# Optimization experiments

Hardware: AMD Instinct MI355X
Metric: run time of the kernel (lower is better)

The kernel has to match this reference:

```python
import jax, jax.numpy as jnp
from jax import lax
import numpy as np

L, B, D_IN, D_OUT, D_MLP = 64, 32, 512, 512, 128
WINDOWS = [1, 3]
FEATS = [256, 128]
C = sum(FEATS)  # 384
EPS = 1e-5


def _leaky(x):
    return jnp.where(x >= 0, x, 0.1 * x)


def setup_inputs() -> dict:
    key = jax.random.key(0)
    ks = jax.random.split(key, 16)
    s = lambda k, shp: (jax.random.normal(k, shp, jnp.float32) * 0.02)
    inp = {}
    inp["x"] = jax.random.normal(ks[0], (L, B, D_IN), jnp.float32)
    inp["xs_mask"] = jnp.ones((L, B), jnp.float32)
    # conv + batchnorm params per window
    inp["conv_w0"] = s(ks[1], (FEATS[0], 1, D_IN * WINDOWS[0]))
    inp["conv_b0"] = jnp.zeros((FEATS[0],), jnp.float32)
    inp["gamma0"] = jnp.ones((FEATS[0],), jnp.float32)
    inp["beta0"] = jnp.zeros((FEATS[0],), jnp.float32)
    inp["conv_w1"] = s(ks[2], (FEATS[1], 1, D_IN * WINDOWS[1]))
    inp["conv_b1"] = jnp.zeros((FEATS[1],), jnp.float32)
    inp["gamma1"] = jnp.ones((FEATS[1],), jnp.float32)
    inp["beta1"] = jnp.zeros((FEATS[1],), jnp.float32)
    inp["w0"] = s(ks[3], (2 * C, D_MLP)); inp["b0"] = jnp.zeros((D_MLP,), jnp.float32)
    inp["w1"] = s(ks[4], (D_MLP, D_MLP)); inp["b1"] = jnp.zeros((D_MLP,), jnp.float32)
    inp["w2"] = s(ks[5], (D_MLP, D_MLP)); inp["b2"] = jnp.zeros((D_MLP,), jnp.float32)
    inp["w3"] = s(ks[6], (D_MLP, D_MLP)); inp["b3"] = jnp.zeros((D_MLP,), jnp.float32)
    # output MLP: Linear(d_mlp->d_mlp), Linear(d_mlp->d_out)
    inp["w4"] = s(ks[7], (D_MLP, D_MLP)); inp["b4"] = jnp.zeros((D_MLP,), jnp.float32)
    inp["w5"] = s(ks[8], (D_MLP, D_OUT)); inp["b5"] = jnp.zeros((D_OUT,), jnp.float32)
    return inp


def reference(x, xs_mask, conv_w0, conv_b0, gamma0, beta0, conv_w1, conv_b1,
              gamma1, beta1, w0, b0, w1, b1, w2, b2, w3, b3, w4, b4, w5, b5):
    # x: (L, B, E)
    x = x * xs_mask[:, :, None]
    xf = jnp.transpose(x, (1, 0, 2)).reshape(B, 1, L * D_IN)  # (B, 1, L*E)

    # CNN front-end: Conv1d(stride=d_in) + BatchNorm1d (batch stats) + LeakyReLU
    feats = []
    for win, cw, cb, g, bt in [(WINDOWS[0], conv_w0, conv_b0, gamma0, beta0),
                               (WINDOWS[1], conv_w1, conv_b1, gamma1, beta1)]:
        pad = (win - 1) // 2 * D_IN
        y = lax.conv_general_dilated(xf, cw, window_strides=(D_IN,),
                                     padding=[(pad, pad)],
                                     dimension_numbers=("NCH", "OIH", "NCH"))
        y = y + cb[None, :, None]  # (B, C_k, L)
        m = y.mean(axis=(0, 2))
        v = y.var(axis=(0, 2))  # biased var, as torch BN training mode
        y = (y - m[None, :, None]) / jnp.sqrt(v[None, :, None] + EPS)
        y = y * g[None, :, None] + bt[None, :, None]
        feats.append(_leaky(y))
    h = jnp.concatenate(feats, axis=1)          # (B, C, L)
    h = jnp.transpose(h, (2, 0, 1))             # (L, B, C)
    h = h * xs_mask[:, :, None]

    # Graph propagation: pairwise concat + first linear, split over concat halves
    # cat([h_i, h_j]) @ w0 == h_i @ w0[:C] + h_j @ w0[C:]  (avoids (L,L,B,2C) tensor)
    a = jnp.einsum("lbc,cd->lbd", h, w0[:C])    # (L, B, d_mlp)
    bb = jnp.einsum("lbc,cd->lbd", h, w0[C:])   # (L, B, d_mlp)
    p = _leaky(a[:, None, :, :] + bb[None, :, :, :] + b0)  # (L, L, B, d_mlp)
    p = _leaky(p @ w1 + b1)
    p = _leaky(p @ w2 + b2)
    p = _leaky(p @ w3 + b3)
    p = p * xs_mask[:, None, :, None]
    p = p.mean(axis=1)                          # (L, B, d_mlp)

    out = _leaky(p @ w4 + b4)
    out = _leaky(out @ w5 + b5)                 # (L, B, d_out)
    return out * xs_mask[:, :, None]
```

## Files before the change

### kernel.cpp

```cpp
#include <hip/hip_runtime.h>


#define BB 32
#define CCH 384

__device__ __forceinline__ float leaky(float x) { return fmaxf(x, 0.1f * x); }

typedef _Float16 f16x8 __attribute__((ext_vector_type(8)));
typedef float f32x4 __attribute__((ext_vector_type(4)));

union F8 { uint4 q; f16x8 h; };
union H2 { _Float16 f[2]; uint32_t u; };

__device__ __forceinline__ void split2(float d0, float d1,
                                       uint32_t& hw, uint32_t& lw) {
  H2 h, l;
  h.f[0] = (_Float16)d0; h.f[1] = (_Float16)d1;
  l.f[0] = (_Float16)((d0 - (float)h.f[0]) * 2048.0f);
  l.f[1] = (_Float16)((d1 - (float)h.f[1]) * 2048.0f);
  hw = h.u; lw = l.u;
}

__global__ __launch_bounds__(256) void conv_kernel(
    const float* __restrict__ x, const float* __restrict__ mask,
    const float* __restrict__ cw0, const float* __restrict__ cw1,
    float* __restrict__ yG, float* __restrict__ Ssum, float* __restrict__ Ssq)
{
  __shared__ uint32_t Ah[64 * 68], Al[64 * 68];
  __shared__ uint32_t Bh[64 * 68], Bl[64 * 68];
  int bx = blockIdx.x;
  int nb = bx % 6, mb = bx / 6;
  int n0 = nb * 64;
  int row0 = mb * 64;
  bool w3 = (nb >= 4);
  int nch = w3 ? 12 : 4;
  const float* wbase = w3 ? (cw1 + (n0 - 256) * 1536) : (cw0 + n0 * 512);
  int wK = w3 ? 1536 : 512;

  int tid = threadIdx.x;
  int wid = __builtin_amdgcn_readfirstlane(tid >> 6);
  int wm = wid & 1, wn2 = wid >> 1;
  int lane = tid & 63;
  int m16 = lane & 15, q = lane >> 4;

  f32x4 hi[2][2], cr[2][2];
#pragma unroll
  for (int a = 0; a < 2; ++a)
#pragma unroll
    for (int b = 0; b < 2; ++b) {
      hi[a][b] = (f32x4){0.f, 0.f, 0.f, 0.f};
      cr[a][b] = (f32x4){0.f, 0.f, 0.f, 0.f};
    }

#pragma unroll 1
  for (int ch = 0; ch < nch; ++ch) {
    int kg0 = ch * 128;
    int tap = kg0 >> 9;
    int d0 = kg0 & 511;
    int shift = w3 ? (tap - 1) * 32 : 0;
    __syncthreads();
#pragma unroll 1
    for (int it = 0; it < 4; ++it) {
      int idx = it * 256 + tid;
      int r = idx >> 4;
      int k8 = (idx & 15) * 8;
      float d[8];
      int rowg = row0 + r + shift;
      if ((unsigned)rowg < 2048u) {
        float mv = mask[rowg];
        const float* xp = x + rowg * 512 + d0 + k8;
        float4 a0 = *(const float4*)xp;
        float4 a1 = *(const float4*)(xp + 4);
        d[0] = a0.x * mv; d[1] = a0.y * mv; d[2] = a0.z * mv; d[3] = a0.w * mv;
        d[4] = a1.x * mv; d[5] = a1.y * mv; d[6] = a1.z * mv; d[7] = a1.w * mv;
      } else {
#pragma unroll
        for (int t2 = 0; t2 < 8; ++t2) d[t2] = 0.f;
      }
      uint4 hq, lq;
      split2(d[0], d[1], hq.x, lq.x);
      split2(d[2], d[3], hq.y, lq.y);
      split2(d[4], d[5], hq.z, lq.z);
      split2(d[6], d[7], hq.w, lq.w);
      *(uint4*)&Ah[r * 68 + k8 / 2] = hq;
      *(uint4*)&Al[r * 68 + k8 / 2] = lq;
      const float* wp = wbase + r * wK + kg0 + k8;
      float4 b0v = *(const float4*)wp;
      float4 b1v = *(const float4*)(wp + 4);
      split2(b0v.x, b0v.y, hq.x, lq.x);
      split2(b0v.z, b0v.w, hq.y, lq.y);
      split2(b1v.x, b1v.y, hq.z, lq.z);
      split2(b1v.z, b1v.w, hq.w, lq.w);
      *(uint4*)&Bh[r * 68 + k8 / 2] = hq;
      *(uint4*)&Bl[r * 68 + k8 / 2] = lq;
    }
    __syncthreads();
#pragma unroll
    for (int ks = 0; ks < 4; ++ks) {
      int koff = ks * 16 + q * 4;
      F8 bh[2], bl[2];
#pragma unroll
      for (int nt = 0; nt < 2; ++nt) {
        int br = wn2 * 32 + nt * 16 + m16;
        bh[nt].q = *(const uint4*)&Bh[br * 68 + koff];
        bl[nt].q = *(const uint4*)&Bl[br * 68 + koff];
      }
#pragma unroll
      for (int mt = 0; mt < 2; ++mt) {
        int ar = wm * 32 + mt * 16 + m16;
        F8 ah, al;
        ah.q = *(const uint4*)&Ah[ar * 68 + koff];
        al.q = *(const uint4*)&Al[ar * 68 + koff];
#pragma unroll
        for (int nt = 0; nt < 2; ++nt) {
          hi[mt][nt] = __builtin_amdgcn_mfma_f32_16x16x32_f16(
              ah.h, bh[nt].h, hi[mt][nt], 0, 0, 0);
          cr[mt][nt] = __builtin_amdgcn_mfma_f32_16x16x32_f16(
              ah.h, bl[nt].h, cr[mt][nt], 0, 0, 0);
          cr[mt][nt] = __builtin_amdgcn_mfma_f32_16x16x32_f16(
              al.h, bh[nt].h, cr[mt][nt], 0, 0, 0);
        }
      }
    }
  }

  float y[2][2][4];
#pragma unroll
  for (int mt = 0; mt < 2; ++mt)
#pragma unroll
    for (int nt = 0; nt < 2; ++nt)
#pragma unroll
      for (int rg = 0; rg < 4; ++rg)
        y[mt][nt][rg] = hi[mt][nt][rg] + cr[mt][nt][rg] * (1.0f / 2048.0f);

#pragma unroll
  for (int nt = 0; nt < 2; ++nt) {
    float s = 0.f, s2 = 0.f;
#pragma unroll
    for (int mt = 0; mt < 2; ++mt)
#pragma unroll
      for (int rg = 0; rg < 4; ++rg) {
        float v = y[mt][nt][rg];
        s += v; s2 += v * v;
      }
    s  += __shfl_xor(s, 16, 64);  s  += __shfl_xor(s, 32, 64);
    s2 += __shfl_xor(s2, 16, 64); s2 += __shfl_xor(s2, 32, 64);
    if (lane < 16) {
      int c = n0 + wn2 * 32 + nt * 16 + m16;
      atomicAdd(&Ssum[c], s);
      atomicAdd(&Ssq[c], s2);
    }
  }

  __syncthreads();
  float* Yl = (float*)Ah;
#pragma unroll
  for (int mt = 0; mt < 2; ++mt)
#pragma unroll
    for (int nt = 0; nt < 2; ++nt)
#pragma unroll
      for (int rg = 0; rg < 4; ++rg)
        Yl[(wn2 * 32 + nt * 16 + m16) * 68 + wm * 32 + mt * 16 + q * 4 + rg] =
            y[mt][nt][rg];
  __syncthreads();
  {
    int c = tid >> 2, seg = (tid & 3) * 16;
#pragma unroll
    for (int j = 0; j < 16; j += 4)
      *(float4*)&yG[(n0 + c) * 2048 + row0 + seg + j] =
          *(const float4*)&Yl[c * 68 + seg + j];
  }
}

__global__ __launch_bounds__(256) void ab_kernel(
    const float* __restrict__ yG, const float* __restrict__ Ssum,
    const float* __restrict__ Ssq,
    const float* __restrict__ g0, const float* __restrict__ be0,
    const float* __restrict__ g1, const float* __restrict__ be1,
    const float* __restrict__ mask, const float* __restrict__ w0,
    const float* __restrict__ w1, const float* __restrict__ w2,
    const float* __restrict__ w3, uint32_t* __restrict__ wpk,
    float* __restrict__ a_arr, float* __restrict__ bb_arr)
{
  int bx = blockIdx.x;
  int tid = threadIdx.x;
  if (bx >= 256) {
    int e = (bx - 256) * 256 + tid;
    int L = e >> 13;
    int r = e & 8191;
    int k2 = r >> 7, n = r & 127;
    int k = k2 * 2;
    const float* w = (L == 0) ? w1 : (L == 1) ? w2 : w3;
    uint32_t hw, lw;
    split2(w[k * 128 + n], w[(k + 1) * 128 + n], hw, lw);
    wpk[L * 8192 + n * 64 + k2] = hw;
    wpk[24576 + L * 8192 + n * 64 + k2] = lw;
    return;
  }
  __shared__ float As[32 * 36];
  __shared__ float Ws[32 * 68];
  __shared__ float scs[384], shs[384];
  for (int c = tid; c < 384; c += 256) {
    float Sv = Ssum[c], S2v = Ssq[c];
    float mean = Sv * (1.f / 2048.f);
    float var  = S2v * (1.f / 2048.f) - mean * mean;
    float g  = (c < 256) ? g0[c] : g1[c - 256];
    float be = (c < 256) ? be0[c] : be1[c - 256];
    float sc = g / sqrtf(var + 1e-5f);
    scs[c] = sc;
    shs[c] = be - mean * sc;
  }
  __syncthreads();

  int rt = bx & 63, ct = bx >> 6;
  int row0 = rt * 32, n0 = ct * 64;
  int r4 = (tid >> 5) * 4;
  int n2 = (tid & 31) * 2;
  int scc = tid >> 3, srr4 = (tid & 7) * 4;
  int wnn8 = (tid & 7) * 8;
  const float* wbase = (n0 < 128) ? (w0 + n0) : (w0 + CCH * 128 + (n0 - 128));
  float4 mv = *(const float4*)(mask + row0 + srr4);

  float acc[4][2] = {{0.f, 0.f}};
#pragma unroll 1
  for (int c0 = 0; c0 < 384; c0 += 32) {
    int c = c0 + scc;
    float4 yv = *(const float4*)(yG + c * 2048 + row0 + srr4);
    float sc = scs[c], sh = shs[c];
    float4 wv0 = *(const float4*)(wbase + c * 128 + wnn8);
    float4 wv1 = *(const float4*)(wbase + c * 128 + wnn8 + 4);
    __syncthreads();
    float4 hv;
    hv.x = leaky(fmaf(yv.x, sc, sh)) * mv.x;
    hv.y = leaky(fmaf(yv.y, sc, sh)) * mv.y;
    hv.z = leaky(fmaf(yv.z, sc, sh)) * mv.z;
    hv.w = leaky(fmaf(yv.w, sc, sh)) * mv.w;
    *(float4*)&As[scc * 36 + srr4] = hv;
    *(float4*)&Ws[scc * 68 + wnn8] = wv0;
    *(float4*)&Ws[scc * 68 + wnn8 + 4] = wv1;
    __syncthreads();
#pragma unroll
    for (int cc = 0; cc < 32; ++cc) {
      float4 a = *(const float4*)&As[cc * 36 + r4];
      float2 w = *(const float2*)&Ws[cc * 68 + n2];
      acc[0][0] = fmaf(a.x, w.x, acc[0][0]); acc[0][1] = fmaf(a.x, w.y, acc[0][1]);
      acc[1][0] = fmaf(a.y, w.x, acc[1][0]); acc[1][1] = fmaf(a.y, w.y, acc[1][1]);
      acc[2][0] = fmaf(a.z, w.x, acc[2][0]); acc[2][1] = fmaf(a.z, w.y, acc[2][1]);
      acc[3][0] = fmaf(a.w, w.x, acc[3][0]); acc[3][1] = fmaf(a.w, w.y, acc[3][1]);
    }
  }
  float* dst; int nd;
  if (n0 < 128) { dst = a_arr; nd = n0; } else { dst = bb_arr; nd = n0 - 128; }
#pragma unroll
  for (int ri = 0; ri < 4; ++ri)
    *(float2*)&dst[(row0 + r4 + ri) * 128 + nd + n2] = make_float2(acc[ri][0], acc[ri][1]);
}

__global__ __launch_bounds__(512) void pair_kernel(
    const float* __restrict__ a_arr, const float* __restrict__ bb_arr,
    const float* __restrict__ b0, const uint32_t* __restrict__ wpk,
    const float* __restrict__ b1, const float* __restrict__ b2,
    const float* __restrict__ b3,
    const float* __restrict__ w4, const float* __restrict__ b4,
    const float* __restrict__ w5, const float* __restrict__ b5,
    const float* __restrict__ mask, float* __restrict__ out)
{
  __shared__ uint32_t Ahs[128 * 68];
  __shared__ uint32_t Als[128 * 68];
  int i = blockIdx.x, bp = blockIdx.y;
  int tid = threadIdx.x;

#pragma unroll 1
  for (int it = 0; it < 4; ++it) {
    int idx = it * 512 + tid;
    int r   = idx >> 4;
    int k8  = (idx & 15) * 8;
    int db  = r >> 6, j = r & 63;
    int bq  = bp * 2 + db;
    const float* ap = a_arr + (i * BB + bq) * 128 + k8;
    const float* bbp = bb_arr + (j * BB + bq) * 128 + k8;
    const float* zp = b0 + k8;
    float d[8];
#pragma unroll
    for (int t = 0; t < 8; t += 4) {
      float4 av = *(const float4*)(ap + t);
      float4 bv = *(const float4*)(bbp + t);
      float4 zv = *(const float4*)(zp + t);
      d[t+0] = leaky(av.x + bv.x + zv.x);
      d[t+1] = leaky(av.y + bv.y + zv.y);
      d[t+2] = leaky(av.z + bv.z + zv.z);
      d[t+3] = leaky(av.w + bv.w + zv.w);
    }
    uint4 hq, lq;
    split2(d[0], d[1], hq.x, lq.x);
    split2(d[2], d[3], hq.y, lq.y);
    split2(d[4], d[5], hq.z, lq.z);
    split2(d[6], d[7], hq.w, lq.w);
    *(uint4*)&Ahs[r * 68 + k8 / 2] = hq;
    *(uint4*)&Als[r * 68 + k8 / 2] = lq;
  }
  __syncthreads();

  int wid = __builtin_amdgcn_readfirstlane(tid >> 6);
  int wm = wid & 1, wn = wid >> 1;
  int lane = tid & 63;
  int m16 = lane & 15, q = lane >> 4;

  f32x4 hi[4][2], cr[4][2];

#pragma unroll 1
  for (int L = 0; L < 3; ++L) {
    const uint32_t* WhL = wpk + L * 8192;
    const uint32_t* WlL = wpk + 24576 + L * 8192;
    const float* Bv = (L == 0) ? b1 : (L == 1) ? b2 : b3;
#pragma unroll
    for (int mt = 0; mt < 4; ++mt)
#pragma unroll
      for (int nt = 0; nt < 2; ++nt) {
        hi[mt][nt] = (f32x4){0.f, 0.f, 0.f, 0.f};
        cr[mt][nt] = (f32x4){0.f, 0.f, 0.f, 0.f};
      }

    F8 Wh[2], Wl[2], Whn[2], Wln[2];
#pragma unroll
    for (int nt = 0; nt < 2; ++nt) {
      int wrow = wn * 32 + nt * 16 + m16;
      Wh[nt].q = *(const uint4*)(WhL + wrow * 64 + q * 4);
      Wl[nt].q = *(const uint4*)(WlL + wrow * 64 + q * 4);
    }

#pragma unroll
    for (int ks = 0; ks < 4; ++ks) {
      int koff2 = ks * 16 + q * 4;
      if (ks < 3) {
#pragma unroll
        for (int nt = 0; nt < 2; ++nt) {
          int wrow = wn * 32 + nt * 16 + m16;
          Whn[nt].q = *(const uint4*)(WhL + wrow * 64 + koff2 + 16);
          Wln[nt].q = *(const uint4*)(WlL + wrow * 64 + koff2 + 16);
        }
      }
#pragma unroll
      for (int mt = 0; mt < 4; ++mt) {
        int arow = wm * 64 + mt * 16 + m16;
        F8 Ah, Al;
        Ah.q = *(const uint4*)&Ahs[arow * 68 + koff2];
        Al.q = *(const uint4*)&Als[arow * 68 + koff2];
#pragma unroll
        for (int nt = 0; nt < 2; ++nt) {
          hi[mt][nt] = __builtin_amdgcn_mfma_f32_16x16x32_f16(
              Ah.h, Wh[nt].h, hi[mt][nt], 0, 0, 0);
          cr[mt][nt] = __builtin_amdgcn_mfma_f32_16x16x32_f16(
              Ah.h, Wl[nt].h, cr[mt][nt], 0, 0, 0);
          cr[mt][nt] = __builtin_amdgcn_mfma_f32_16x16x32_f16(
              Al.h, Wh[nt].h, cr[mt][nt], 0, 0, 0);
        }
      }
#pragma unroll
      for (int nt = 0; nt < 2; ++nt) { Wh[nt] = Whn[nt]; Wl[nt] = Wln[nt]; }
    }

    float bias[2];
#pragma unroll
    for (int nt = 0; nt < 2; ++nt) bias[nt] = Bv[wn * 32 + nt * 16 + m16];

    if (L < 2) {
      __syncthreads();
      int par = lane & 1;
#pragma unroll
      for (int mt = 0; mt < 4; ++mt)
#pragma unroll
        for (int nt = 0; nt < 2; ++nt) {
          int colw = (wn * 32 + nt * 16 + (m16 & ~1)) >> 1;
#pragma unroll
          for (int rg = 0; rg < 4; ++rg) {
            float d = leaky(hi[mt][nt][rg] + cr[mt][nt][rg] * (1.0f / 2048.0f)
                            + bias[nt]);
            float dn = __shfl_xor(d, 1, 64);
            float de = par ? dn : d;
            float do_ = par ? d : dn;
            uint32_t hw, lw;
            split2(de, do_, hw, lw);
            int row = wm * 64 + mt * 16 + q * 4 + rg;
            if (par) Als[row * 68 + colw] = lw;
            else     Ahs[row * 68 + colw] = hw;
          }
        }
      __syncthreads();
    } else {
      float s[2] = {0.f, 0.f};
#pragma unroll
      for (int nt = 0; nt < 2; ++nt)
#pragma unroll
        for (int mt = 0; mt < 4; ++mt)
#pragma unroll
          for (int rg = 0; rg < 4; ++rg)
            s[nt] += leaky(hi[mt][nt][rg] + cr[mt][nt][rg] * (1.0f / 2048.0f)
                           + bias[nt]);
      int browp = i * BB + bp * 2 + wm;
      float mfac = (1.0f / 64.0f) * mask[browp];
#pragma unroll
      for (int nt = 0; nt < 2; ++nt) {
        s[nt] += __shfl_xor(s[nt], 16, 64);
        s[nt] += __shfl_xor(s[nt], 32, 64);
      }
      __syncthreads();
      float* scratch = (float*)Ahs;
      float* Pm = scratch;
      float* Tp = scratch + 256;
      float* T4 = scratch + 768;
      if (lane < 16) {
#pragma unroll
        for (int nt = 0; nt < 2; ++nt)
          Pm[wm * 128 + wn * 32 + nt * 16 + m16] = s[nt] * mfac;
      }
      __syncthreads();
      {
        int row = tid >> 8;
        int chh = (tid >> 7) & 1;
        int k   = tid & 127;
        const float* pm  = Pm + row * 128 + chh * 64;
        const float* w4c = w4 + chh * 64 * 128 + k;
        float t = chh ? 0.f : b4[k];
#pragma unroll 4
        for (int c0 = 0; c0 < 64; c0 += 4) {
          float4 pv = *(const float4*)&pm[c0];
          t = fmaf(pv.x, w4c[(c0 + 0) * 128], t);
          t = fmaf(pv.y, w4c[(c0 + 1) * 128], t);
          t = fmaf(pv.z, w4c[(c0 + 2) * 128], t);
          t = fmaf(pv.w, w4c[(c0 + 3) * 128], t);
        }
        Tp[(row * 2 + chh) * 128 + k] = t;
      }
      __syncthreads();
      if (tid < 256) {
        int row = tid >> 7, k = tid & 127;
        T4[row * 128 + k] = leaky(Tp[row * 256 + k] + Tp[row * 256 + 128 + k]);
      }
      __syncthreads();
      {
        int kk = tid;
        float o0 = b5[kk], o1 = o0;
#pragma unroll 4
        for (int c0 = 0; c0 < 128; c0 += 4) {
          float4 ta = *(const float4*)&T4[c0];
          float4 tb = *(const float4*)&T4[128 + c0];
          float w0v = w5[(c0 + 0) * 512 + kk];
          float w1v = w5[(c0 + 1) * 512 + kk];
          float w2v = w5[(c0 + 2) * 512 + kk];
          float w3v = w5[(c0 + 3) * 512 + kk];
          o0 = fmaf(ta.x, w0v, o0); o1 = fmaf(tb.x, w0v, o1);
          o0 = fmaf(ta.y, w1v, o0); o1 = fmaf(tb.y, w1v, o1);
          o0 = fmaf(ta.z, w2v, o0); o1 = fmaf(tb.z, w2v, o1);
          o0 = fmaf(ta.w, w3v, o0); o1 = fmaf(tb.w, w3v, o1);
        }
        int brow0 = i * BB + bp * 2;
        float m0 = mask[brow0], m1 = mask[brow0 + 1];
        out[brow0 * 512 + kk]       = leaky(o0) * m0;
        out[(brow0 + 1) * 512 + kk] = leaky(o1) * m1;
      }
    }
  }
}

extern "C" void kernel_launch(void* const* d_in, const int* in_sizes, int n_in,
                              void* d_out, int out_size, void* d_ws, size_t ws_size,
                              hipStream_t stream) {
  const float* x    = (const float*)d_in[0];
  const float* mask = (const float*)d_in[1];
  const float* cw0  = (const float*)d_in[2];
  const float* g0   = (const float*)d_in[4];
  const float* be0  = (const float*)d_in[5];
  const float* cw1  = (const float*)d_in[6];
  const float* g1   = (const float*)d_in[8];
  const float* be1  = (const float*)d_in[9];
  const float* w0   = (const float*)d_in[10];
  const float* b0   = (const float*)d_in[11];
  const float* w1   = (const float*)d_in[12];
  const float* b1   = (const float*)d_in[13];
  const float* w2   = (const float*)d_in[14];
  const float* b2   = (const float*)d_in[15];
  const float* w3   = (const float*)d_in[16];
  const float* b3   = (const float*)d_in[17];
  const float* w4   = (const float*)d_in[18];
  const float* b4   = (const float*)d_in[19];
  const float* w5   = (const float*)d_in[20];
  const float* b5   = (const float*)d_in[21];

  float* ws     = (float*)d_ws;
  float* Ssum   = ws;
  float* Ssq    = ws + 384;
  float* yG     = ws + 768;
  uint32_t* wpk = (uint32_t*)(ws + 787200);
  float* a_arr  = ws + 836352;
  float* bb_arr = ws + 1098496;
  float* outp   = (float*)d_out;

  hipMemsetAsync(Ssum, 0, 768 * sizeof(float), stream);
  conv_kernel<<<192, 256, 0, stream>>>(x, mask, cw0, cw1, yG, Ssum, Ssq);
  ab_kernel<<<352, 256, 0, stream>>>(yG, Ssum, Ssq, g0, be0, g1, be1,
                                     mask, w0, w1, w2, w3, wpk, a_arr, bb_arr);
  dim3 g5(64, 16);
  pair_kernel<<<g5, 512, 0, stream>>>(a_arr, bb_arr, b0, wpk, b1, b2, b3,
                                      w4, b4, w5, b5, mask, outp);
}
```

Before: 259.3 us.

## Split pair kernel to one batch per block, halving tile and LDS

Each pair_kernel block now handles a single batch element (64 pair rows) instead of two, so the grid doubles to 64x32 and the shared-memory tiles, accumulator arrays and per-wave M tiles are halved. launch_bounds adds a minimum-occupancy hint so more blocks can be resident per CU. The a-row plus bias is loaded once per thread and reused across the j rows. The output MLP tail is restructured for a single row, with the w4 reduction split four ways. In exchange, weight fragments are reloaded from global memory twice as often in total, and each block does less MFMA work to hide its fixed overhead.

```diff
diff --git a/kernel.cpp b/kernel.cpp
--- a/kernel.cpp
+++ b/kernel.cpp
@@ -256,7 +256,7 @@
     *(float2*)&dst[(row0 + r4 + ri) * 128 + nd + n2] = make_float2(acc[ri][0], acc[ri][1]);
 }
 
-__global__ __launch_bounds__(512) void pair_kernel(
+__global__ __launch_bounds__(512, 6) void pair_kernel(
     const float* __restrict__ a_arr, const float* __restrict__ bb_arr,
     const float* __restrict__ b0, const uint32_t* __restrict__ wpk,
     const float* __restrict__ b1, const float* __restrict__ b2,
@@ -265,39 +265,45 @@
     const float* __restrict__ w5, const float* __restrict__ b5,
     const float* __restrict__ mask, float* __restrict__ out)
 {
-  __shared__ uint32_t Ahs[128 * 68];
-  __shared__ uint32_t Als[128 * 68];
-  int i = blockIdx.x, bp = blockIdx.y;
+  __shared__ uint32_t Ahs[64 * 68];
+  __shared__ uint32_t Als[64 * 68];
+  int i = blockIdx.x, b = blockIdx.y;
   int tid = threadIdx.x;
-
-#pragma unroll 1
-  for (int it = 0; it < 4; ++it) {
-    int idx = it * 512 + tid;
-    int r   = idx >> 4;
-    int k8  = (idx & 15) * 8;
-    int db  = r >> 6, j = r & 63;
-    int bq  = bp * 2 + db;
-    const float* ap = a_arr + (i * BB + bq) * 128 + k8;
-    const float* bbp = bb_arr + (j * BB + bq) * 128 + k8;
+  int browp = i * BB + b;
+
+  {
+    int k8 = (tid & 15) * 8;
+    const float* ap = a_arr + browp * 128 + k8;
     const float* zp = b0 + k8;
-    float d[8];
+    float az[8];
 #pragma unroll
     for (int t = 0; t < 8; t += 4) {
       float4 av = *(const float4*)(ap + t);
-      float4 bv = *(const float4*)(bbp + t);
       float4 zv = *(const float4*)(zp + t);
-      d[t+0] = leaky(av.x + bv.x + zv.x);
-      d[t+1] = leaky(av.y + bv.y + zv.y);
-      d[t+2] = leaky(av.z + bv.z + zv.z);
-      d[t+3] = leaky(av.w + bv.w + zv.w);
-    }
-    uint4 hq, lq;
-    split2(d[0], d[1], hq.x, lq.x);
-    split2(d[2], d[3], hq.y, lq.y);
-    split2(d[4], d[5], hq.z, lq.z);
-    split2(d[6], d[7], hq.w, lq.w);
-    *(uint4*)&Ahs[r * 68 + k8 / 2] = hq;
-    *(uint4*)&Als[r * 68 + k8 / 2] = lq;
+      az[t + 0] = av.x + zv.x; az[t + 1] = av.y + zv.y;
+      az[t + 2] = av.z + zv.z; az[t + 3] = av.w + zv.w;
+    }
+#pragma unroll
+    for (int it = 0; it < 2; ++it) {
+      int r = (it * 512 + tid) >> 4;
+      const float* bbp = bb_arr + (r * BB + b) * 128 + k8;
+      float d[8];
+#pragma unroll
+      for (int t = 0; t < 8; t += 4) {
+        float4 bv = *(const float4*)(bbp + t);
+        d[t + 0] = leaky(az[t + 0] + bv.x);
+        d[t + 1] = leaky(az[t + 1] + bv.y);
+        d[t + 2] = leaky(az[t + 2] + bv.z);
+        d[t + 3] = leaky(az[t + 3] + bv.w);
+      }
+      uint4 hq, lq;
+      split2(d[0], d[1], hq.x, lq.x);
+      split2(d[2], d[3], hq.y, lq.y);
+      split2(d[4], d[5], hq.z, lq.z);
+      split2(d[6], d[7], hq.w, lq.w);
+      *(uint4*)&Ahs[r * 68 + k8 / 2] = hq;
+      *(uint4*)&Als[r * 68 + k8 / 2] = lq;
+    }
   }
   __syncthreads();
 
@@ -306,7 +312,7 @@
   int lane = tid & 63;
   int m16 = lane & 15, q = lane >> 4;
 
-  f32x4 hi[4][2], cr[4][2];
+  f32x4 hi[2][2], cr[2][2];
 
 #pragma unroll 1
   for (int L = 0; L < 3; ++L) {
@@ -314,7 +320,7 @@
     const uint32_t* WlL = wpk + 24576 + L * 8192;
     const float* Bv = (L == 0) ? b1 : (L == 1) ? b2 : b3;
 #pragma unroll
-    for (int mt = 0; mt < 4; ++mt)
+    for (int mt = 0; mt < 2; ++mt)
 #pragma unroll
       for (int nt = 0; nt < 2; ++nt) {
         hi[mt][nt] = (f32x4){0.f, 0.f, 0.f, 0.f};
@@ -341,8 +347,8 @@
         }
       }
 #pragma unroll
-      for (int mt = 0; mt < 4; ++mt) {
-        int arow = wm * 64 + mt * 16 + m16;
+      for (int mt = 0; mt < 2; ++mt) {
+        int arow = wm * 32 + mt * 16 + m16;
         F8 Ah, Al;
         Ah.q = *(const uint4*)&Ahs[arow * 68 + koff2];
         Al.q = *(const uint4*)&Als[arow * 68 + koff2];
@@ -368,7 +374,7 @@
       __syncthreads();
       int par = lane & 1;
 #pragma unroll
-      for (int mt = 0; mt < 4; ++mt)
+      for (int mt = 0; mt < 2; ++mt)
 #pragma unroll
         for (int nt = 0; nt < 2; ++nt) {
           int colw = (wn * 32 + nt * 16 + (m16 & ~1)) >> 1;
@@ -381,7 +387,7 @@
             float do_ = par ? d : dn;
             uint32_t hw, lw;
             split2(de, do_, hw, lw);
-            int row = wm * 64 + mt * 16 + q * 4 + rg;
+            int row = wm * 32 + mt * 16 + q * 4 + rg;
             if (par) Als[row * 68 + colw] = lw;
             else     Ahs[row * 68 + colw] = hw;
           }
@@ -392,12 +398,11 @@
 #pragma unroll
       for (int nt = 0; nt < 2; ++nt)
 #pragma unroll
-        for (int mt = 0; mt < 4; ++mt)
+        for (int mt = 0; mt < 2; ++mt)
 #pragma unroll
           for (int rg = 0; rg < 4; ++rg)
             s[nt] += leaky(hi[mt][nt][rg] + cr[mt][nt][rg] * (1.0f / 2048.0f)
                            + bias[nt]);
-      int browp = i * BB + bp * 2 + wm;
       float mfac = (1.0f / 64.0f) * mask[browp];
 #pragma unroll
       for (int nt = 0; nt < 2; ++nt) {
@@ -407,57 +412,48 @@
       __syncthreads();
       float* scratch = (float*)Ahs;
       float* Pm = scratch;
-      float* Tp = scratch + 256;
-      float* T4 = scratch + 768;
+      float* Pc = scratch + 256;
+      float* Tp = scratch + 384;
+      float* T4 = scratch + 896;
       if (lane < 16) {
 #pragma unroll
         for (int nt = 0; nt < 2; ++nt)
           Pm[wm * 128 + wn * 32 + nt * 16 + m16] = s[nt] * mfac;
       }
       __syncthreads();
+      if (tid < 128) Pc[tid] = Pm[tid] + Pm[128 + tid];
+      __syncthreads();
       {
-        int row = tid >> 8;
-        int chh = (tid >> 7) & 1;
-        int k   = tid & 127;
-        const float* pm  = Pm + row * 128 + chh * 64;
-        const float* w4c = w4 + chh * 64 * 128 + k;
-        float t = chh ? 0.f : b4[k];
-#pragma unroll 4
-        for (int c0 = 0; c0 < 64; c0 += 4) {
-          float4 pv = *(const float4*)&pm[c0];
+        int k = tid & 127, chh = tid >> 7;
+        const float* w4c = w4 + (chh * 32) * 128 + k;
+        const float* pc = Pc + chh * 32;
+        float t = 0.f;
+#pragma unroll 8
+        for (int c0 = 0; c0 < 32; c0 += 4) {
+          float4 pv = *(const float4*)&pc[c0];
           t = fmaf(pv.x, w4c[(c0 + 0) * 128], t);
           t = fmaf(pv.y, w4c[(c0 + 1) * 128], t);
           t = fmaf(pv.z, w4c[(c0 + 2) * 128], t);
           t = fmaf(pv.w, w4c[(c0 + 3) * 128], t);
         }
-        Tp[(row * 2 + chh) * 128 + k] = t;
-      }
-      __syncthreads();
-      if (tid < 256) {
-        int row = tid >> 7, k = tid & 127;
-        T4[row * 128 + k] = leaky(Tp[row * 256 + k] + Tp[row * 256 + 128 + k]);
-      }
+        Tp[chh * 128 + k] = t;
+      }
+      __syncthreads();
+      if (tid < 128)
+        T4[tid] = leaky(Tp[tid] + Tp[128 + tid] + Tp[256 + tid] +
+                        Tp[384 + tid] + b4[tid]);
       __syncthreads();
       {
-        int kk = tid;
-        float o0 = b5[kk], o1 = o0;
+        float o = b5[tid];
 #pragma unroll 4
         for (int c0 = 0; c0 < 128; c0 += 4) {
-          float4 ta = *(const float4*)&T4[c0];
-          float4 tb = *(const float4*)&T4[128 + c0];
-          float w0v = w5[(c0 + 0) * 512 + kk];
-          float w1v = w5[(c0 + 1) * 512 + kk];
-          float w2v = w5[(c0 + 2) * 512 + kk];
-          float w3v = w5[(c0 + 3) * 512 + kk];
-          o0 = fmaf(ta.x, w0v, o0); o1 = fmaf(tb.x, w0v, o1);
-          o0 = fmaf(ta.y, w1v, o0); o1 = fmaf(tb.y, w1v, o1);
-          o0 = fmaf(ta.z, w2v, o0); o1 = fmaf(tb.z, w2v, o1);
-          o0 = fmaf(ta.w, w3v, o0); o1 = fmaf(tb.w, w3v, o1);
+          float4 tv = *(const float4*)&T4[c0];
+          o = fmaf(tv.x, w5[(c0 + 0) * 512 + tid], o);
+          o = fmaf(tv.y, w5[(c0 + 1) * 512 + tid], o);
+          o = fmaf(tv.z, w5[(c0 + 2) * 512 + tid], o);
+          o = fmaf(tv.w, w5[(c0 + 3) * 512 + tid], o);
         }
-        int brow0 = i * BB + bp * 2;
-        float m0 = mask[brow0], m1 = mask[brow0 + 1];
-        out[brow0 * 512 + kk]       = leaky(o0) * m0;
-        out[(brow0 + 1) * 512 + kk] = leaky(o1) * m1;
+        out[browp * 512 + tid] = leaky(o) * mask[browp];
       }
     }
   }
@@ -500,7 +496,7 @@
   conv_kernel<<<192, 256, 0, stream>>>(x, mask, cw0, cw1, yG, Ssum, Ssq);
   ab_kernel<<<352, 256, 0, stream>>>(yG, Ssum, Ssq, g0, be0, g1, be1,
                                      mask, w0, w1, w2, w3, wpk, a_arr, bb_arr);
-  dim3 g5(64, 16);
+  dim3 g5(64, 32);
   pair_kernel<<<g5, 512, 0, stream>>>(a_arr, bb_arr, b0, wpk, b1, b2, b3,
                                       w4, b4, w5, b5, mask, outp);
 }
```

Result: slower. 421.2 us (+62.4%).
